# Optimization experiments

Hardware: AMD Instinct MI355X
Metric: run time of the kernel (lower is better)

Reference implementation:

```python
import jax, jax.numpy as jnp
import numpy as np

N0, N1, N2 = 100000, 20000, 4000
DEG = 10
G_NODES = 200000
D, ED, CD, FF, NHEAD = 512, 256, 300, 2048, 2


def _layernorm(x, g, b, eps=1e-5):
    m = jnp.mean(x, -1, keepdims=True)
    v = jnp.var(x, -1, keepdims=True)
    return (x - m) * jax.lax.rsqrt(v + eps) * g + b


def _mha(q_in, kv_in, w_in, b_in, w_out, b_out):
    # torch nn.MultiheadAttention, inputs are (seq, batch, d)
    d = q_in.shape[-1]
    wq, wk, wv = w_in[:d], w_in[d:2 * d], w_in[2 * d:]
    bq, bk, bv = b_in[:d], b_in[d:2 * d], b_in[2 * d:]
    dh = d // NHEAD
    q = (q_in @ wq.T + bq).reshape(q_in.shape[0], q_in.shape[1], NHEAD, dh)
    k = (kv_in @ wk.T + bk).reshape(kv_in.shape[0], kv_in.shape[1], NHEAD, dh)
    v = (kv_in @ wv.T + bv).reshape(kv_in.shape[0], kv_in.shape[1], NHEAD, dh)
    scores = jnp.einsum('qnhd,knhd->nhqk', q, k) * (dh ** -0.5)
    o = jnp.einsum('nhqk,knhd->qnhd', jax.nn.softmax(scores, -1), v)
    o = o.reshape(q_in.shape[0], q_in.shape[1], d)
    return o @ w_out.T + b_out


def setup_inputs() -> dict:
    key = jax.random.key(0)
    k = lambda i: jax.random.fold_in(key, i)
    inp = {}
    inp['nid0'] = jax.random.randint(k(0), (N0,), 0, G_NODES, dtype=jnp.int32)
    inp['nid1'] = jax.random.randint(k(1), (N1,), 0, G_NODES, dtype=jnp.int32)
    inp['nid2'] = jax.random.randint(k(2), (N2,), 0, G_NODES, dtype=jnp.int32)
    inp['esrc0'] = jax.random.randint(k(3), (N1 * DEG,), 0, N0, dtype=jnp.int32)
    inp['edst0'] = jnp.repeat(jnp.arange(N1, dtype=jnp.int32), DEG)
    inp['esrc1'] = jax.random.randint(k(4), (N2 * DEG,), 0, N1, dtype=jnp.int32)
    inp['edst1'] = jnp.repeat(jnp.arange(N2, dtype=jnp.int32), DEG)
    inp['content0'] = jax.random.normal(k(5), (N0, CD), jnp.float32)
    inp['content1'] = jax.random.normal(k(6), (N1, CD), jnp.float32)
    inp['content2'] = jax.random.normal(k(7), (N2, CD), jnp.float32)
    inp['node_emb_w'] = jax.random.normal(k(8), (G_NODES + 1, ED), jnp.float32) / ED
    inp['ee_w'] = jax.random.normal(k(9), (D, ED), jnp.float32) * 0.06
    inp['ee_b'] = jax.random.normal(k(10), (D,), jnp.float32) * 0.001
    inp['proj_w'] = jax.random.normal(k(11), (D, CD), jnp.float32) * 0.06
    inp['proj_b'] = jax.random.normal(k(12), (D,), jnp.float32) * 0.001
    inp['proj_g'] = jnp.ones((D,), jnp.float32)
    inp['proj_beta'] = jnp.zeros((D,), jnp.float32)
    L = 2  # decoder layers
    inp['sa_in_w'] = jax.random.normal(k(13), (L, 3 * D, D), jnp.float32) * 0.04
    inp['sa_in_b'] = jnp.zeros((L, 3 * D), jnp.float32)
    inp['sa_out_w'] = jax.random.normal(k(14), (L, D, D), jnp.float32) * 0.04
    inp['sa_out_b'] = jnp.zeros((L, D), jnp.float32)
    inp['ca_in_w'] = jax.random.normal(k(15), (L, 3 * D, D), jnp.float32) * 0.04
    inp['ca_in_b'] = jnp.zeros((L, 3 * D), jnp.float32)
    inp['ca_out_w'] = jax.random.normal(k(16), (L, D, D), jnp.float32) * 0.04
    inp['ca_out_b'] = jnp.zeros((L, D), jnp.float32)
    inp['lin1_w'] = jax.random.normal(k(17), (L, FF, D), jnp.float32) * 0.03
    inp['lin1_b'] = jnp.zeros((L, FF), jnp.float32)
    inp['lin2_w'] = jax.random.normal(k(18), (L, D, FF), jnp.float32) * 0.03
    inp['lin2_b'] = jnp.zeros((L, D), jnp.float32)
    for n in ('n1', 'n2', 'n3'):
        inp[n + '_g'] = jnp.ones((L, D), jnp.float32)
        inp[n + '_b'] = jnp.zeros((L, D), jnp.float32)
    return inp


def _forward(nid0, nid1, nid2, esrc0, edst0, esrc1, edst1,
             content0, content1, content2, node_emb_w, ee_w, ee_b,
             proj_w, proj_b, proj_g, proj_beta,
             sa_in_w, sa_in_b, sa_out_w, sa_out_b,
             ca_in_w, ca_in_b, ca_out_w, ca_out_b,
             lin1_w, lin1_b, lin2_w, lin2_b,
             n1_g, n1_b, n2_g, n2_b, n3_g, n3_b):
    def node_h(nid, content):
        nh = node_emb_w[nid + 1] @ ee_w.T + ee_b           # emb_expand(node_emb(nid+1))
        c = _layernorm(jax.nn.leaky_relu(content @ proj_w.T + proj_b, 0.1), proj_g, proj_beta)
        h = nh + c                                          # mix_embeddings (c[:, :D] == c)
        return h / jnp.maximum(jnp.linalg.norm(h, axis=1, keepdims=True), 1e-5)

    h0 = node_h(nid0, content0)
    h1 = node_h(nid1, content1)
    h2 = node_h(nid2, content2)

    def agg_mean(h_src, src, dst, n_dst):
        s = jax.ops.segment_sum(h_src[src], dst, num_segments=n_dst)
        w = jax.ops.segment_sum(jnp.ones(src.shape[0], h_src.dtype), dst, num_segments=n_dst)
        return s / w[:, None]

    # block 0: non-prediction GraphConv -> concat(mean_agg, h), L2 normalize
    m1 = agg_mean(h0, esrc0, edst0, N1)
    h1 = jnp.concatenate([m1, h1], axis=1)                  # (N1, 2D)
    h1 = h1 / jnp.maximum(jnp.linalg.norm(h1, axis=1, keepdims=True), 1e-5)

    # block 1: prediction GraphConv -> transformer-decoder fusion
    m2 = agg_mean(h1, esrc1, edst1, N2)                     # (N2, 2D)
    mem = m2.reshape(N2, 2, D).transpose(1, 0, 2)           # (n_layer=2, N2, D)
    tgt = h2[None]                                          # (1, N2, D)
    for l in range(2):  # post-norm TransformerDecoderLayer, gelu, dropout=0
        t2 = _mha(tgt, tgt, sa_in_w[l], sa_in_b[l], sa_out_w[l], sa_out_b[l])
        tgt = _layernorm(tgt + t2, n1_g[l], n1_b[l])
        t2 = _mha(tgt, mem, ca_in_w[l], ca_in_b[l], ca_out_w[l], ca_out_b[l])
        tgt = _layernorm(tgt + t2, n2_g[l], n2_b[l])
        ff = jax.nn.gelu(tgt @ lin1_w[l].T + lin1_b[l], approximate=False) @ lin2_w[l].T + lin2_b[l]
        tgt = _layernorm(tgt + ff, n3_g[l], n3_b[l])
    out = tgt[0]                                            # squeeze -> (N2, D)
    return out / jnp.maximum(jnp.linalg.norm(out, axis=1, keepdims=True), 1e-5)


def reference(nid0, nid1, nid2, esrc0, edst0, esrc1, edst1,
              content0, content1, content2, node_emb_w, ee_w, ee_b,
              proj_w, proj_b, proj_g, proj_beta,
              sa_in_w, sa_in_b, sa_out_w, sa_out_b,
              ca_in_w, ca_in_b, ca_out_w, ca_out_b,
              lin1_w, lin1_b, lin2_w, lin2_b,
              n1_g, n1_b, n2_g, n2_b, n3_g, n3_b):
    return _forward(nid0, nid1, nid2, esrc0, edst0, esrc1, edst1,
                    content0, content1, content2, node_emb_w, ee_w, ee_b,
                    proj_w, proj_b, proj_g, proj_beta,
                    sa_in_w, sa_in_b, sa_out_w, sa_out_b,
                    ca_in_w, ca_in_b, ca_out_w, ca_out_b,
                    lin1_w, lin1_b, lin2_w, lin2_b,
                    n1_g, n1_b, n2_g, n2_b, n3_g, n3_b)
```

## Files before the change

kernel.cpp:

```cpp
#include <hip/hip_runtime.h>
#include <math.h>

static constexpr int kN0  = 100000;
static constexpr int kN1  = 20000;
static constexpr int kN2  = 4000;
static constexpr int kDeg = 10;
static constexpr int kD   = 512;
static constexpr int kFF  = 2048;
static constexpr int kRows  = 48;
static constexpr int kRowsN = 32;
static constexpr int kLdA  = 584;
static constexpr int kLdG  = 520;

using short8  = __attribute__((ext_vector_type(8))) short;
using floatx4 = __attribute__((ext_vector_type(4))) float;

__device__ inline unsigned short f2bf(float f) {
    union { float f; unsigned u; } v; v.f = f;
    unsigned r = v.u + 0x7FFFu + ((v.u >> 16) & 1u);
    return (unsigned short)(r >> 16);
}
__device__ inline float bf2f(ushort u) {
    union { unsigned v; float f; } x; x.v = (unsigned)u << 16; return x.f;
}

__global__ __launch_bounds__(256) void pack_node_w_kernel(
    const float* __restrict__ ee_w, const float* __restrict__ proj_w,
    ushort* __restrict__ Bp)
{
    int tid  = blockIdx.x * 256 + threadIdx.x;
    int lane = tid & 63;
    int tile = tid >> 6;
    int n     = (tile & 31) * 16 + (lane & 15);
    int kbase = (tile >> 5) * 32 + (lane >> 4) * 8;
    ushort v[8];
    #pragma unroll
    for (int j = 0; j < 8; ++j) {
        int k = kbase + j;
        float f = 0.f;
        if (k < 256)      f = ee_w[(size_t)n * 256 + k];
        else if (k < 556) f = proj_w[(size_t)n * 300 + (k - 256)];
        v[j] = f2bf(f);
    }
    uint4 u;
    u.x = (unsigned)v[0] | ((unsigned)v[1] << 16);
    u.y = (unsigned)v[2] | ((unsigned)v[3] << 16);
    u.z = (unsigned)v[4] | ((unsigned)v[5] << 16);
    u.w = (unsigned)v[6] | ((unsigned)v[7] << 16);
    *(uint4*)(Bp + (size_t)tid * 8) = u;
}

__global__ __launch_bounds__(256) void pack512_many_kernel(
    const float* __restrict__ sa_in_w, const float* __restrict__ sa_out_w,
    const float* __restrict__ ca_in_w, const float* __restrict__ ca_out_w,
    ushort* __restrict__ dst)
{
    int y = blockIdx.y, l = y / 6, m = y % 6;
    const float* W;
    switch (m) {
        case 0: W = sa_in_w  + (size_t)l * 3 * kD * kD + (size_t)2 * kD * kD; break;
        case 1: W = sa_out_w + (size_t)l * kD * kD; break;
        case 2: W = ca_in_w  + (size_t)l * 3 * kD * kD; break;
        case 3: W = ca_in_w  + (size_t)l * 3 * kD * kD + (size_t)kD * kD; break;
        case 4: W = ca_in_w  + (size_t)l * 3 * kD * kD + (size_t)2 * kD * kD; break;
        default:W = ca_out_w + (size_t)l * kD * kD; break;
    }
    int tid  = blockIdx.x * 256 + threadIdx.x;
    int lane = tid & 63;
    int tile = tid >> 6;
    int n  = (tile & 31) * 16 + (lane & 15);
    int kb = (tile >> 5) * 32 + (lane >> 4) * 8;
    const float* src = W + (size_t)n * 512 + kb;
    ushort v[8];
    #pragma unroll
    for (int j = 0; j < 8; ++j) v[j] = f2bf(src[j]);
    uint4 u;
    u.x = (unsigned)v[0] | ((unsigned)v[1] << 16);
    u.y = (unsigned)v[2] | ((unsigned)v[3] << 16);
    u.z = (unsigned)v[4] | ((unsigned)v[5] << 16);
    u.w = (unsigned)v[6] | ((unsigned)v[7] << 16);
    *(uint4*)(dst + (size_t)y * 262144 + (size_t)tid * 8) = u;
}

__global__ __launch_bounds__(256) void pack_generic_kernel(
    const float* __restrict__ src, size_t srcStride,
    ushort* __restrict__ dst, size_t dstStride, int N, int K)
{
    int tid  = blockIdx.x * 256 + threadIdx.x;
    int NT = N >> 4;
    int lane = tid & 63;
    int tile = tid >> 6;
    int ct = tile % NT, kc = tile / NT;
    int n  = ct * 16 + (lane & 15);
    int kb = kc * 32 + (lane >> 4) * 8;
    const float* W = src + blockIdx.y * srcStride + (size_t)n * K + kb;
    ushort v[8];
    #pragma unroll
    for (int j = 0; j < 8; ++j) v[j] = f2bf(W[j]);
    uint4 u;
    u.x = (unsigned)v[0] | ((unsigned)v[1] << 16);
    u.y = (unsigned)v[2] | ((unsigned)v[3] << 16);
    u.z = (unsigned)v[4] | ((unsigned)v[5] << 16);
    u.w = (unsigned)v[6] | ((unsigned)v[7] << 16);
    *(uint4*)(dst + blockIdx.y * dstStride + (size_t)tid * 8) = u;
}

__global__ __launch_bounds__(512, 4) void node_h_mfma(
    const int* __restrict__ nid0a, const float* __restrict__ content0a,
    ushort* __restrict__ outB0, int n0,
    const int* __restrict__ nid1a, const float* __restrict__ content1a,
    ushort* __restrict__ outB1, int n1,
    const int* __restrict__ nid2a, const float* __restrict__ content2a,
    ushort* __restrict__ outB2, float* __restrict__ outF2, int n2,
    const float* __restrict__ node_emb_w,
    const ushort* __restrict__ Bp,
    const float* __restrict__ ee_b, const float* __restrict__ proj_b,
    const float* __restrict__ proj_g, const float* __restrict__ proj_beta)
{
    __shared__ __align__(16) ushort As[kRowsN * kLdA];
    __shared__ float redS[8][kRowsN], redQ[8][kRowsN];
    __shared__ float meanv[kRowsN], rstdv[kRowsN], rowinv[kRowsN];

    const int t    = threadIdx.x;
    const int lane = t & 63;
    const int wv   = t >> 6;
    const int quad = lane >> 4;
    const int l15  = lane & 15;

    const int g0 = (n0 + kRowsN - 1) / kRowsN;
    const int g1 = (n1 + kRowsN - 1) / kRowsN;
    int bx = blockIdx.x;
    const int* nid; const float* content; ushort* outB; float* outF = nullptr;
    int ldh, n;
    if (bx < g0)           { nid = nid0a; content = content0a; outB = outB0; ldh = 512;  n = n0; }
    else if (bx < g0 + g1) { bx -= g0; nid = nid1a; content = content1a; outB = outB1; ldh = 1024; n = n1; }
    else                   { bx -= g0 + g1; nid = nid2a; content = content2a; outB = outB2; outF = outF2; ldh = 512; n = n2; }
    const int row0 = bx * kRowsN;

    #pragma unroll
    for (int it = 0; it < 9; ++it) {
        int flat = it * 512 + t;
        int r  = flat / 144;
        int k4 = flat - r * 144;
        int row = row0 + r; if (row >= n) row = n - 1;
        float4 f = make_float4(0.f, 0.f, 0.f, 0.f);
        if (k4 < 64)
            f = *(const float4*)(node_emb_w + ((size_t)(nid[row] + 1)) * 256 + k4 * 4);
        else if (k4 < 139)
            f = *(const float4*)(content + (size_t)row * 300 + (k4 - 64) * 4);
        ushort4 o = make_ushort4(f2bf(f.x), f2bf(f.y), f2bf(f.z), f2bf(f.w));
        *(ushort4*)(As + (size_t)r * kLdA + k4 * 4) = o;
    }
    __syncthreads();

    floatx4 acc[2][4] = {};
    const short8* BpV = (const short8*)Bp;

    #pragma unroll
    for (int kc = 8; kc < 18; ++kc) {
        const short8* bp = BpV + (size_t)(kc * 32 + wv * 4) * 64 + lane;
        short8 b0 = bp[0], b1 = bp[64], b2 = bp[128], b3 = bp[192];
        short8 a[2];
        #pragma unroll
        for (int rt = 0; rt < 2; ++rt)
            a[rt] = *(const short8*)(As + (size_t)(rt * 16 + l15) * kLdA + kc * 32 + quad * 8);
        #pragma unroll
        for (int rt = 0; rt < 2; ++rt) {
            acc[rt][0] = __builtin_amdgcn_mfma_f32_16x16x32_bf16(a[rt], b0, acc[rt][0], 0, 0, 0);
            acc[rt][1] = __builtin_amdgcn_mfma_f32_16x16x32_bf16(a[rt], b1, acc[rt][1], 0, 0, 0);
            acc[rt][2] = __builtin_amdgcn_mfma_f32_16x16x32_bf16(a[rt], b2, acc[rt][2], 0, 0, 0);
            acc[rt][3] = __builtin_amdgcn_mfma_f32_16x16x32_bf16(a[rt], b3, acc[rt][3], 0, 0, 0);
        }
    }

    const int colbase = wv * 64 + l15;
    float pb[4], pg[4], pbt[4], eb[4];
    #pragma unroll
    for (int ct = 0; ct < 4; ++ct) {
        int c = colbase + ct * 16;
        pb[ct]  = proj_b[c];
        pg[ct]  = proj_g[c];
        pbt[ct] = proj_beta[c];
        eb[ct]  = ee_b[c];
    }

    float s8[8], q8[8];
    #pragma unroll
    for (int rt = 0; rt < 2; ++rt) {
        #pragma unroll
        for (int i = 0; i < 4; ++i) {
            float s = 0.f, q = 0.f;
            #pragma unroll
            for (int ct = 0; ct < 4; ++ct) {
                float c = acc[rt][ct][i] + pb[ct];
                c = (c >= 0.f) ? c : 0.1f * c;
                acc[rt][ct][i] = c;
                s += c; q = fmaf(c, c, q);
            }
            s8[rt * 4 + i] = s; q8[rt * 4 + i] = q;
        }
    }
    #pragma unroll
    for (int idx = 0; idx < 8; ++idx) {
        #pragma unroll
        for (int m = 1; m < 16; m <<= 1) {
            s8[idx] += __shfl_xor(s8[idx], m);
            q8[idx] += __shfl_xor(q8[idx], m);
        }
    }
    if (l15 == 0) {
        #pragma unroll
        for (int rt = 0; rt < 2; ++rt)
            #pragma unroll
            for (int i = 0; i < 4; ++i) {
                int rl = rt * 16 + quad * 4 + i;
                redS[wv][rl] = s8[rt * 4 + i];
                redQ[wv][rl] = q8[rt * 4 + i];
            }
    }
    __syncthreads();
    if (t < kRowsN) {
        float s = 0.f, q = 0.f;
        #pragma unroll
        for (int w = 0; w < 8; ++w) { s += redS[w][t]; q += redQ[w][t]; }
        float m   = s * (1.f / 512.f);
        float var = q * (1.f / 512.f) - m * m;
        meanv[t] = m;
        rstdv[t] = rsqrtf(var + 1e-5f);
    }
    __syncthreads();

    #pragma unroll
    for (int rt = 0; rt < 2; ++rt) {
        #pragma unroll
        for (int i = 0; i < 4; ++i) {
            int rl = rt * 16 + quad * 4 + i;
            float m = meanv[rl], rs = rstdv[rl];
            #pragma unroll
            for (int ct = 0; ct < 4; ++ct)
                acc[rt][ct][i] = (acc[rt][ct][i] - m) * rs * pg[ct] + pbt[ct] + eb[ct];
        }
    }

    #pragma unroll
    for (int kc = 0; kc < 8; ++kc) {
        const short8* bp = BpV + (size_t)(kc * 32 + wv * 4) * 64 + lane;
        short8 b0 = bp[0], b1 = bp[64], b2 = bp[128], b3 = bp[192];
        short8 a[2];
        #pragma unroll
        for (int rt = 0; rt < 2; ++rt)
            a[rt] = *(const short8*)(As + (size_t)(rt * 16 + l15) * kLdA + kc * 32 + quad * 8);
        #pragma unroll
        for (int rt = 0; rt < 2; ++rt) {
            acc[rt][0] = __builtin_amdgcn_mfma_f32_16x16x32_bf16(a[rt], b0, acc[rt][0], 0, 0, 0);
            acc[rt][1] = __builtin_amdgcn_mfma_f32_16x16x32_bf16(a[rt], b1, acc[rt][1], 0, 0, 0);
            acc[rt][2] = __builtin_amdgcn_mfma_f32_16x16x32_bf16(a[rt], b2, acc[rt][2], 0, 0, 0);
            acc[rt][3] = __builtin_amdgcn_mfma_f32_16x16x32_bf16(a[rt], b3, acc[rt][3], 0, 0, 0);
        }
    }

    #pragma unroll
    for (int rt = 0; rt < 2; ++rt) {
        #pragma unroll
        for (int i = 0; i < 4; ++i) {
            float psq = 0.f;
            #pragma unroll
            for (int ct = 0; ct < 4; ++ct)
                psq = fmaf(acc[rt][ct][i], acc[rt][ct][i], psq);
            q8[rt * 4 + i] = psq;
        }
    }
    #pragma unroll
    for (int idx = 0; idx < 8; ++idx)
        #pragma unroll
        for (int m = 1; m < 16; m <<= 1)
            q8[idx] += __shfl_xor(q8[idx], m);
    if (l15 == 0) {
        #pragma unroll
        for (int rt = 0; rt < 2; ++rt)
            #pragma unroll
            for (int i = 0; i < 4; ++i)
                redS[wv][rt * 16 + quad * 4 + i] = q8[rt * 4 + i];
    }
    __syncthreads();
    if (t < kRowsN) {
        float s = 0.f;
        #pragma unroll
        for (int w = 0; w < 8; ++w) s += redS[w][t];
        rowinv[t] = 1.f / fmaxf(sqrtf(s), 1e-5f);
    }
    __syncthreads();

    #pragma unroll
    for (int rt = 0; rt < 2; ++rt) {
        #pragma unroll
        for (int i = 0; i < 4; ++i) {
            int rl = rt * 16 + quad * 4 + i;
            int grow = row0 + rl;
            if (grow < n) {
                float inv = rowinv[rl];
                ushort* dB = outB + (size_t)grow * ldh + colbase;
                #pragma unroll
                for (int ct = 0; ct < 4; ++ct) {
                    float v = acc[rt][ct][i] * inv;
                    dB[ct * 16] = f2bf(v);
                    if (outF) outF[(size_t)grow * ldh + colbase + ct * 16] = v;
                }
            }
        }
    }
}

__device__ inline float gelu_exact(float x) {
    return 0.5f * x * (1.f + erff(x * 0.70710678118654752f));
}

template<int EPI>
__global__ __launch_bounds__(512, 2) void gemm_mfma(
    const ushort* __restrict__ A, int lda,
    const ushort* __restrict__ Bp, const float* __restrict__ bias,
    ushort* __restrict__ Cb, float* __restrict__ Cf, int ldc,
    const float* __restrict__ resid,
    const float* __restrict__ lng, const float* __restrict__ lnb,
    int M, int K, int N)
{
    __shared__ __align__(16) ushort As[kRows * kLdG];
    __shared__ float redS[8][kRows], redQ[8][kRows];
    __shared__ float meanv[kRows], rstdv[kRows];

    const int t    = threadIdx.x;
    const int lane = t & 63;
    const int wv   = t >> 6;
    const int quad = lane >> 4;
    const int l15  = lane & 15;
    const int row0 = blockIdx.x * kRows;
    const int nb   = blockIdx.y;
    const int NT   = N >> 4;

    floatx4 acc[3][4] = {};
    const short8* BpV = (const short8*)Bp;

    for (int k0 = 0; k0 < K; k0 += 512) {
        #pragma unroll
        for (int it = 0; it < 6; ++it) {
            int flat = it * 512 + t;
            int r  = flat >> 6;
            int k8 = flat & 63;
            int row = row0 + r; if (row >= M) row = M - 1;
            short8 v = *(const short8*)(A + (size_t)row * lda + k0 + k8 * 8);
            *(short8*)(As + (size_t)r * kLdG + k8 * 8) = v;
        }
        __syncthreads();
        const int g0 = k0 >> 5;
        #pragma unroll
        for (int kc = 0; kc < 16; ++kc) {
            const short8* bp = BpV + ((size_t)(g0 + kc) * NT + nb * 32 + wv * 4) * 64 + lane;
            short8 b0 = bp[0], b1 = bp[64], b2 = bp[128], b3 = bp[192];
            short8 a[3];
            #pragma unroll
            for (int rt = 0; rt < 3; ++rt)
                a[rt] = *(const short8*)(As + (size_t)(rt * 16 + l15) * kLdG + kc * 32 + quad * 8);
            #pragma unroll
            for (int rt = 0; rt < 3; ++rt) {
                acc[rt][0] = __builtin_amdgcn_mfma_f32_16x16x32_bf16(a[rt], b0, acc[rt][0], 0, 0, 0);
                acc[rt][1] = __builtin_amdgcn_mfma_f32_16x16x32_bf16(a[rt], b1, acc[rt][1], 0, 0, 0);
                acc[rt][2] = __builtin_amdgcn_mfma_f32_16x16x32_bf16(a[rt], b2, acc[rt][2], 0, 0, 0);
                acc[rt][3] = __builtin_amdgcn_mfma_f32_16x16x32_bf16(a[rt], b3, acc[rt][3], 0, 0, 0);
            }
        }
        __syncthreads();
    }

    const int colloc = wv * 64 + l15;
    float b[4];
    #pragma unroll
    for (int ct = 0; ct < 4; ++ct) b[ct] = bias[nb * 512 + colloc + ct * 16];

    if constexpr (EPI == 0 || EPI == 1) {
        #pragma unroll
        for (int rt = 0; rt < 3; ++rt) {
            #pragma unroll
            for (int i = 0; i < 4; ++i) {
                int row = row0 + rt * 16 + quad * 4 + i;
                if (row < M) {
                    ushort* dst = Cb + (size_t)row * ldc + nb * 512 + colloc;
                    #pragma unroll
                    for (int ct = 0; ct < 4; ++ct) {
                        float v = acc[rt][ct][i] + b[ct];
                        if (EPI == 1) v = gelu_exact(v);
                        dst[ct * 16] = f2bf(v);
                    }
                }
            }
        }
    } else {
        float lg[4], lb[4];
        #pragma unroll
        for (int ct = 0; ct < 4; ++ct) {
            lg[ct] = lng[colloc + ct * 16];
            lb[ct] = lnb[colloc + ct * 16];
        }
        float s12[12], q12[12];
        #pragma unroll
        for (int rt = 0; rt < 3; ++rt) {
            #pragma unroll
            for (int i = 0; i < 4; ++i) {
                int rl = rt * 16 + quad * 4 + i;
                int row = row0 + rl; if (row >= M) row = M - 1;
                const float* rr = resid + (size_t)row * 512 + colloc;
                float s = 0.f, q = 0.f;
                #pragma unroll
                for (int ct = 0; ct < 4; ++ct) {
                    float h = acc[rt][ct][i] + b[ct] + rr[ct * 16];
                    acc[rt][ct][i] = h;
                    s += h; q = fmaf(h, h, q);
                }
                s12[rt * 4 + i] = s; q12[rt * 4 + i] = q;
            }
        }
        #pragma unroll
        for (int idx = 0; idx < 12; ++idx) {
            #pragma unroll
            for (int m = 1; m < 16; m <<= 1) {
                s12[idx] += __shfl_xor(s12[idx], m);
                q12[idx] += __shfl_xor(q12[idx], m);
            }
        }
        if (l15 == 0) {
            #pragma unroll
            for (int rt = 0; rt < 3; ++rt)
                #pragma unroll
                for (int i = 0; i < 4; ++i) {
                    int rl = rt * 16 + quad * 4 + i;
                    redS[wv][rl] = s12[rt * 4 + i];
                    redQ[wv][rl] = q12[rt * 4 + i];
                }
        }
        __syncthreads();
        if (t < kRows) {
            float s = 0.f, q = 0.f;
            #pragma unroll
            for (int w = 0; w < 8; ++w) { s += redS[w][t]; q += redQ[w][t]; }
            float m   = s * (1.f / 512.f);
            float var = q * (1.f / 512.f) - m * m;
            meanv[t] = m;
            rstdv[t] = rsqrtf(var + 1e-5f);
        }
        __syncthreads();
        #pragma unroll
        for (int rt = 0; rt < 3; ++rt) {
            #pragma unroll
            for (int i = 0; i < 4; ++i) {
                int rl = rt * 16 + quad * 4 + i;
                int row = row0 + rl;
                if (row < M) {
                    float m = meanv[rl], rs = rstdv[rl];
                    float*  dF = Cf + (size_t)row * 512 + colloc;
                    ushort* dB = Cb + (size_t)row * 512 + colloc;
                    #pragma unroll
                    for (int ct = 0; ct < 4; ++ct) {
                        float v = (acc[rt][ct][i] - m) * rs * lg[ct] + lb[ct];
                        dF[ct * 16] = v;
                        dB[ct * 16] = f2bf(v);
                    }
                }
            }
        }
    }
}

__global__ __launch_bounds__(512, 2) void gemm3_mfma(
    const ushort* __restrict__ A0, const ushort* __restrict__ B0,
    const float* __restrict__ b0p, ushort* __restrict__ C0, int M0,
    const ushort* __restrict__ A1, const ushort* __restrict__ B1,
    const float* __restrict__ b1p, ushort* __restrict__ C1, int M1,
    const ushort* __restrict__ A2, const ushort* __restrict__ B2,
    const float* __restrict__ b2p, ushort* __restrict__ C2, int M2)
{
    __shared__ __align__(16) ushort As[kRows * kLdG];

    const int t    = threadIdx.x;
    const int lane = t & 63;
    const int wv   = t >> 6;
    const int quad = lane >> 4;
    const int l15  = lane & 15;

    const int g0 = (M0 + kRows - 1) / kRows;
    const int g1 = (M1 + kRows - 1) / kRows;
    int bx = blockIdx.x;
    const ushort* A; const ushort* Bw; const float* bias; ushort* C; int M;
    if (bx < g0)           { A = A0; Bw = B0; bias = b0p; C = C0; M = M0; }
    else if (bx < g0 + g1) { bx -= g0; A = A1; Bw = B1; bias = b1p; C = C1; M = M1; }
    else                   { bx -= g0 + g1; A = A2; Bw = B2; bias = b2p; C = C2; M = M2; }
    const int row0 = bx * kRows;

    floatx4 acc[3][4] = {};
    const short8* BpV = (const short8*)Bw;

    #pragma unroll
    for (int it = 0; it < 6; ++it) {
        int flat = it * 512 + t;
        int r  = flat >> 6;
        int k8 = flat & 63;
        int row = row0 + r; if (row >= M) row = M - 1;
        short8 v = *(const short8*)(A + (size_t)row * 512 + k8 * 8);
        *(short8*)(As + (size_t)r * kLdG + k8 * 8) = v;
    }
    __syncthreads();
    #pragma unroll
    for (int kc = 0; kc < 16; ++kc) {
        const short8* bp = BpV + ((size_t)kc * 32 + wv * 4) * 64 + lane;
        short8 b0 = bp[0], b1 = bp[64], b2 = bp[128], b3 = bp[192];
        short8 a[3];
        #pragma unroll
        for (int rt = 0; rt < 3; ++rt)
            a[rt] = *(const short8*)(As + (size_t)(rt * 16 + l15) * kLdG + kc * 32 + quad * 8);
        #pragma unroll
        for (int rt = 0; rt < 3; ++rt) {
            acc[rt][0] = __builtin_amdgcn_mfma_f32_16x16x32_bf16(a[rt], b0, acc[rt][0], 0, 0, 0);
            acc[rt][1] = __builtin_amdgcn_mfma_f32_16x16x32_bf16(a[rt], b1, acc[rt][1], 0, 0, 0);
            acc[rt][2] = __builtin_amdgcn_mfma_f32_16x16x32_bf16(a[rt], b2, acc[rt][2], 0, 0, 0);
            acc[rt][3] = __builtin_amdgcn_mfma_f32_16x16x32_bf16(a[rt], b3, acc[rt][3], 0, 0, 0);
        }
    }

    const int colloc = wv * 64 + l15;
    float b[4];
    #pragma unroll
    for (int ct = 0; ct < 4; ++ct) b[ct] = bias[colloc + ct * 16];
    #pragma unroll
    for (int rt = 0; rt < 3; ++rt) {
        #pragma unroll
        for (int i = 0; i < 4; ++i) {
            int row = row0 + rt * 16 + quad * 4 + i;
            if (row < M) {
                ushort* dst = C + (size_t)row * 512 + colloc;
                #pragma unroll
                for (int ct = 0; ct < 4; ++ct)
                    dst[ct * 16] = f2bf(acc[rt][ct][i] + b[ct]);
            }
        }
    }
}

__device__ inline float block_sum256(float v, float* red4) {
    #pragma unroll
    for (int off = 32; off > 0; off >>= 1) v += __shfl_down(v, off);
    if ((threadIdx.x & 63) == 0) red4[threadIdx.x >> 6] = v;
    __syncthreads();
    return red4[0] + red4[1] + red4[2] + red4[3];
}

__global__ __launch_bounds__(256) void agg_norm1_kernel(
    const ushort* __restrict__ h0, const int* __restrict__ esrc,
    ushort* __restrict__ h1cat)
{
    __shared__ int idx[kDeg];
    __shared__ float red4[4];
    int i = blockIdx.x, t = threadIdx.x;
    if (t < kDeg) idx[t] = esrc[i * kDeg + t];
    __syncthreads();
    float s0 = 0.f, s1 = 0.f;
    for (int e = 0; e < kDeg; ++e) {
        const ushort* hr = h0 + (size_t)idx[e] * 512;
        s0 += bf2f(hr[t]); s1 += bf2f(hr[t + 256]);
    }
    s0 *= 0.1f; s1 *= 0.1f;
    size_t base = (size_t)i * 1024;
    float o0 = bf2f(h1cat[base + 512 + t]);
    float o1 = bf2f(h1cat[base + 768 + t]);
    float tot = block_sum256(s0 * s0 + s1 * s1 + o0 * o0 + o1 * o1, red4);
    float inv = 1.f / fmaxf(sqrtf(tot), 1e-5f);
    h1cat[base + t]       = f2bf(s0 * inv);
    h1cat[base + 256 + t] = f2bf(s1 * inv);
    h1cat[base + 512 + t] = f2bf(o0 * inv);
    h1cat[base + 768 + t] = f2bf(o1 * inv);
}

__global__ __launch_bounds__(256) void agg2_kernel(
    const ushort* __restrict__ h1cat, const int* __restrict__ esrc,
    ushort* __restrict__ m2)
{
    __shared__ int idx[kDeg];
    int i = blockIdx.x, t = threadIdx.x;
    if (t < kDeg) idx[t] = esrc[i * kDeg + t];
    __syncthreads();
    float s0 = 0.f, s1 = 0.f, s2 = 0.f, s3 = 0.f;
    for (int e = 0; e < kDeg; ++e) {
        const ushort* hr = h1cat + (size_t)idx[e] * 1024;
        s0 += bf2f(hr[t]);       s1 += bf2f(hr[t + 256]);
        s2 += bf2f(hr[t + 512]); s3 += bf2f(hr[t + 768]);
    }
    size_t base = (size_t)i * 1024;
    m2[base + t]       = f2bf(s0 * 0.1f);
    m2[base + 256 + t] = f2bf(s1 * 0.1f);
    m2[base + 512 + t] = f2bf(s2 * 0.1f);
    m2[base + 768 + t] = f2bf(s3 * 0.1f);
}

__global__ __launch_bounds__(256) void attn_combine_kernel(
    const ushort* __restrict__ Q,
    const ushort* __restrict__ Kb, const ushort* __restrict__ Vb,
    ushort* __restrict__ O)
{
    __shared__ float red[4][4];
    __shared__ float a[4];
    int i = blockIdx.x, t = threadIdx.x;
    size_t base  = (size_t)i * 512;
    size_t base0 = (size_t)(2 * i) * 512;
    size_t base1 = base0 + 512;
    float q0 = bf2f(Q[base + t]), q1 = bf2f(Q[base + t + 256]);
    float p00 = q0 * bf2f(Kb[base0 + t]);
    float p01 = q0 * bf2f(Kb[base1 + t]);
    float p10 = q1 * bf2f(Kb[base0 + t + 256]);
    float p11 = q1 * bf2f(Kb[base1 + t + 256]);
    #pragma unroll
    for (int off = 32; off > 0; off >>= 1) {
        p00 += __shfl_down(p00, off);
        p01 += __shfl_down(p01, off);
        p10 += __shfl_down(p10, off);
        p11 += __shfl_down(p11, off);
    }
    int w = t >> 6;
    if ((t & 63) == 0) { red[w][0] = p00; red[w][1] = p01; red[w][2] = p10; red[w][3] = p11; }
    __syncthreads();
    if (t == 0) {
        float s00 = (red[0][0] + red[1][0] + red[2][0] + red[3][0]) * 0.0625f;
        float s01 = (red[0][1] + red[1][1] + red[2][1] + red[3][1]) * 0.0625f;
        float s10 = (red[0][2] + red[1][2] + red[2][2] + red[3][2]) * 0.0625f;
        float s11 = (red[0][3] + red[1][3] + red[2][3] + red[3][3]) * 0.0625f;
        float m0 = fmaxf(s00, s01);
        float e0 = expf(s00 - m0), e1 = expf(s01 - m0);
        float d0 = e0 + e1;
        a[0] = e0 / d0; a[1] = e1 / d0;
        float m1 = fmaxf(s10, s11);
        float f0 = expf(s10 - m1), f1 = expf(s11 - m1);
        float d1 = f0 + f1;
        a[2] = f0 / d1; a[3] = f1 / d1;
    }
    __syncthreads();
    O[base + t]       = f2bf(a[0] * bf2f(Vb[base0 + t])       + a[1] * bf2f(Vb[base1 + t]));
    O[base + t + 256] = f2bf(a[2] * bf2f(Vb[base0 + t + 256]) + a[3] * bf2f(Vb[base1 + t + 256]));
}

__global__ __launch_bounds__(256) void final_norm_kernel(
    const float* __restrict__ tgt, float* __restrict__ out)
{
    __shared__ float red4[4];
    int i = blockIdx.x, t = threadIdx.x;
    size_t base = (size_t)i * 512;
    float v0 = tgt[base + t], v1 = tgt[base + t + 256];
    float tot = block_sum256(v0 * v0 + v1 * v1, red4);
    float inv = 1.f / fmaxf(sqrtf(tot), 1e-5f);
    out[base + t]       = v0 * inv;
    out[base + t + 256] = v1 * inv;
}

extern "C" void kernel_launch(void* const* d_in, const int* in_sizes, int n_in,
                              void* d_out, int out_size, void* d_ws, size_t ws_size,
                              hipStream_t stream)
{
    (void)in_sizes; (void)n_in; (void)out_size; (void)ws_size;
    const int*   nid0       = (const int*)d_in[0];
    const int*   nid1       = (const int*)d_in[1];
    const int*   nid2       = (const int*)d_in[2];
    const int*   esrc0      = (const int*)d_in[3];
    const int*   esrc1      = (const int*)d_in[5];
    const float* content0   = (const float*)d_in[7];
    const float* content1   = (const float*)d_in[8];
    const float* content2   = (const float*)d_in[9];
    const float* node_emb_w = (const float*)d_in[10];
    const float* ee_w       = (const float*)d_in[11];
    const float* ee_b       = (const float*)d_in[12];
    const float* proj_w     = (const float*)d_in[13];
    const float* proj_b     = (const float*)d_in[14];
    const float* proj_g     = (const float*)d_in[15];
    const float* proj_beta  = (const float*)d_in[16];
    const float* sa_in_w    = (const float*)d_in[17];
    const float* sa_in_b    = (const float*)d_in[18];
    const float* sa_out_w   = (const float*)d_in[19];
    const float* sa_out_b   = (const float*)d_in[20];
    const float* ca_in_w    = (const float*)d_in[21];
    const float* ca_in_b    = (const float*)d_in[22];
    const float* ca_out_w   = (const float*)d_in[23];
    const float* ca_out_b   = (const float*)d_in[24];
    const float* lin1_w     = (const float*)d_in[25];
    const float* lin1_b     = (const float*)d_in[26];
    const float* lin2_w     = (const float*)d_in[27];
    const float* lin2_b     = (const float*)d_in[28];
    const float* n1_g       = (const float*)d_in[29];
    const float* n1_b       = (const float*)d_in[30];
    const float* n2_g       = (const float*)d_in[31];
    const float* n2_b       = (const float*)d_in[32];
    const float* n3_g       = (const float*)d_in[33];
    const float* n3_b       = (const float*)d_in[34];

    float* ws = (float*)d_ws;
    size_t off = 0;
    ushort* h0b    = (ushort*)(ws + off); off += (size_t)kN0 * 512 / 2;
    ushort* h1catb = (ushort*)(ws + off); off += (size_t)kN1 * 1024 / 2;
    ushort* m2b    = (ushort*)(ws + off); off += (size_t)kN2 * 1024 / 2;
    float*  tgt    = ws + off;            off += (size_t)kN2 * 512;
    ushort* tgtb   = (ushort*)(ws + off); off += (size_t)kN2 * 512 / 2;
    ushort* Qbb    = (ushort*)(ws + off); off += (size_t)kN2 * 512 / 2;
    ushort* Kbb    = (ushort*)(ws + off); off += (size_t)2 * kN2 * 512 / 2;
    ushort* Vbb    = (ushort*)(ws + off); off += (size_t)2 * kN2 * 512 / 2;
    ushort* Obb    = (ushort*)(ws + off); off += (size_t)kN2 * 512 / 2;
    ushort* ffhb   = (ushort*)(ws + off); off += (size_t)kN2 * 2048 / 2;
    ushort* BpNode = (ushort*)(ws + off); off += 147456;
    ushort* Pw512  = (ushort*)(ws + off); off += 12 * 262144 / 2;
    ushort* Pl1    = (ushort*)(ws + off); off += 2 * 1048576 / 2;
    ushort* Pl2    = (ushort*)(ws + off); off += 2 * 1048576 / 2;

    dim3 blk(256);

    pack_node_w_kernel<<<dim3(144), blk, 0, stream>>>(ee_w, proj_w, BpNode);
    pack512_many_kernel<<<dim3(128, 12), blk, 0, stream>>>(
        sa_in_w, sa_out_w, ca_in_w, ca_out_w, Pw512);
    pack_generic_kernel<<<dim3(512, 2), blk, 0, stream>>>(
        lin1_w, (size_t)kFF * kD, Pl1, 1048576, kFF, kD);
    pack_generic_kernel<<<dim3(512, 2), blk, 0, stream>>>(
        lin2_w, (size_t)kD * kFF, Pl2, 1048576, kD, kFF);

    {
        int g0 = (kN0 + kRowsN - 1) / kRowsN;
        int g1 = (kN1 + kRowsN - 1) / kRowsN;
        int g2 = (kN2 + kRowsN - 1) / kRowsN;
        node_h_mfma<<<dim3(g0 + g1 + g2), dim3(512), 0, stream>>>(
            nid0, content0, h0b, kN0,
            nid1, content1, h1catb + 512, kN1,
            nid2, content2, tgtb, tgt, kN2,
            node_emb_w, BpNode, ee_b, proj_b, proj_g, proj_beta);
    }

    agg_norm1_kernel<<<dim3(kN1), blk, 0, stream>>>(h0b, esrc0, h1catb);
    agg2_kernel<<<dim3(kN2), blk, 0, stream>>>(h1catb, esrc1, m2b);

    const int M   = kN2;
    const int gM  = (M + kRows - 1) / kRows;
    const int gM2 = (2 * M + kRows - 1) / kRows;
    dim3 blk512(512);
    for (int l = 0; l < 2; ++l) {
        const ushort* sa_v_p   = Pw512 + (size_t)(l * 6 + 0) * 262144;
        const ushort* sa_out_p = Pw512 + (size_t)(l * 6 + 1) * 262144;
        const ushort* ca_q_p   = Pw512 + (size_t)(l * 6 + 2) * 262144;
        const ushort* ca_k_p   = Pw512 + (size_t)(l * 6 + 3) * 262144;
        const ushort* ca_v_p   = Pw512 + (size_t)(l * 6 + 4) * 262144;
        const ushort* ca_out_p = Pw512 + (size_t)(l * 6 + 5) * 262144;
        const ushort* l1_p     = Pl1 + (size_t)l * 1048576;
        const ushort* l2_p     = Pl2 + (size_t)l * 1048576;
        const float* sa_b = sa_in_b + (size_t)l * 3 * kD;
        const float* saob = sa_out_b + (size_t)l * kD;
        const float* ca_b = ca_in_b + (size_t)l * 3 * kD;
        const float* caob = ca_out_b + (size_t)l * kD;
        const float* l1b = lin1_b + (size_t)l * kFF;
        const float* l2b = lin2_b + (size_t)l * kD;

        gemm3_mfma<<<dim3(gM + gM2 + gM2), blk512, 0, stream>>>(
            tgtb, sa_v_p, sa_b + 2 * kD, Qbb, M,
            m2b,  ca_k_p, ca_b + kD,     Kbb, 2 * M,
            m2b,  ca_v_p, ca_b + 2 * kD, Vbb, 2 * M);

        gemm_mfma<2><<<dim3(gM, 1), blk512, 0, stream>>>(
            Qbb, 512, sa_out_p, saob, tgtb, tgt, 512,
            tgt, n1_g + l * kD, n1_b + l * kD, M, 512, 512);

        gemm_mfma<0><<<dim3(gM, 1), blk512, 0, stream>>>(
            tgtb, 512, ca_q_p, ca_b, Qbb, nullptr, 512,
            nullptr, nullptr, nullptr, M, 512, 512);
        attn_combine_kernel<<<dim3(M), blk, 0, stream>>>(Qbb, Kbb, Vbb, Obb);
        gemm_mfma<2><<<dim3(gM, 1), blk512, 0, stream>>>(
            Obb, 512, ca_out_p, caob, tgtb, tgt, 512,
            tgt, n2_g + l * kD, n2_b + l * kD, M, 512, 512);

        gemm_mfma<1><<<dim3(gM, 4), blk512, 0, stream>>>(
            tgtb, 512, l1_p, l1b, ffhb, nullptr, 2048,
            nullptr, nullptr, nullptr, M, 512, 2048);
        gemm_mfma<2><<<dim3(gM, 1), blk512, 0, stream>>>(
            ffhb, 2048, l2_p, l2b, tgtb, tgt, 512,
            tgt, n3_g + l * kD, n3_b + l * kD, M, 2048, 512);
    }

    final_norm_kernel<<<dim3(kN2), blk, 0, stream>>>(tgt, (float*)d_out);
}
```

Measured before the change: 961.0 us.

## Fuse follow-on projections into LayerNorm GEMM epilogues and hoist cross-attn K/V

Adds an EPI==3 variant of the GEMM. After the LayerNorm epilogue it writes the normalised bf16 row tile into shared memory and multiplies it by a second 512x512 weight, producing the next projection (cross-attn Q, or the next layer's self-attn V) in the same launch. Cross-attention K/V for both layers depend only on m2b, so they are computed once up front in a single 5-way batched GEMM launch. The node_h_mfma launch bound is raised to 8 waves per SIMD. Together these cut kernel launches and re-reads of tgtb, at the cost of extra buffers and more register pressure from the second accumulator.

```diff
diff --git a/kernel.cpp b/kernel.cpp
--- a/kernel.cpp
+++ b/kernel.cpp
@@ -105,7 +105,7 @@
     *(uint4*)(dst + blockIdx.y * dstStride + (size_t)tid * 8) = u;
 }
 
-__global__ __launch_bounds__(512, 4) void node_h_mfma(
+__global__ __launch_bounds__(512, 8) void node_h_mfma(
     const int* __restrict__ nid0a, const float* __restrict__ content0a,
     ushort* __restrict__ outB0, int n0,
     const int* __restrict__ nid1a, const float* __restrict__ content1a,
@@ -322,7 +322,9 @@
     ushort* __restrict__ Cb, float* __restrict__ Cf, int ldc,
     const float* __restrict__ resid,
     const float* __restrict__ lng, const float* __restrict__ lnb,
-    int M, int K, int N)
+    int M, int K, int N,
+    const ushort* __restrict__ Bp2, const float* __restrict__ bias2,
+    ushort* __restrict__ C2)
 {
     __shared__ __align__(16) ushort As[kRows * kLdG];
     __shared__ float redS[8][kRows], redQ[8][kRows];
@@ -462,20 +464,63 @@
                         float v = (acc[rt][ct][i] - m) * rs * lg[ct] + lb[ct];
                         dF[ct * 16] = v;
                         dB[ct * 16] = f2bf(v);
+                        if (EPI == 3)
+                            As[(size_t)rl * kLdG + colloc + ct * 16] = f2bf(v);
                     }
                 }
             }
         }
-    }
-}
-
-__global__ __launch_bounds__(512, 2) void gemm3_mfma(
-    const ushort* __restrict__ A0, const ushort* __restrict__ B0,
+        if constexpr (EPI == 3) {
+            __syncthreads();
+            floatx4 acc2[3][4] = {};
+            const short8* Bp2V = (const short8*)Bp2;
+            #pragma unroll
+            for (int kc = 0; kc < 16; ++kc) {
+                const short8* bp = Bp2V + ((size_t)kc * 32 + wv * 4) * 64 + lane;
+                short8 b0 = bp[0], b1 = bp[64], b2 = bp[128], b3 = bp[192];
+                short8 a[3];
+                #pragma unroll
+                for (int rt = 0; rt < 3; ++rt)
+                    a[rt] = *(const short8*)(As + (size_t)(rt * 16 + l15) * kLdG + kc * 32 + quad * 8);
+                #pragma unroll
+                for (int rt = 0; rt < 3; ++rt) {
+                    acc2[rt][0] = __builtin_amdgcn_mfma_f32_16x16x32_bf16(a[rt], b0, acc2[rt][0], 0, 0, 0);
+                    acc2[rt][1] = __builtin_amdgcn_mfma_f32_16x16x32_bf16(a[rt], b1, acc2[rt][1], 0, 0, 0);
+                    acc2[rt][2] = __builtin_amdgcn_mfma_f32_16x16x32_bf16(a[rt], b2, acc2[rt][2], 0, 0, 0);
+                    acc2[rt][3] = __builtin_amdgcn_mfma_f32_16x16x32_bf16(a[rt], b3, acc2[rt][3], 0, 0, 0);
+                }
+            }
+            float b2[4];
+            #pragma unroll
+            for (int ct = 0; ct < 4; ++ct) b2[ct] = bias2[colloc + ct * 16];
+            #pragma unroll
+            for (int rt = 0; rt < 3; ++rt) {
+                #pragma unroll
+                for (int i = 0; i < 4; ++i) {
+                    int row = row0 + rt * 16 + quad * 4 + i;
+                    if (row < M) {
+                        ushort* dst = C2 + (size_t)row * 512 + colloc;
+                        #pragma unroll
+                        for (int ct = 0; ct < 4; ++ct)
+                            dst[ct * 16] = f2bf(acc2[rt][ct][i] + b2[ct]);
+                    }
+                }
+            }
+        }
+    }
+}
+
+__global__ __launch_bounds__(512, 2) void gemm5_mfma(
+    const ushort* __restrict__ A0, const ushort* __restrict__ B0w,
     const float* __restrict__ b0p, ushort* __restrict__ C0, int M0,
-    const ushort* __restrict__ A1, const ushort* __restrict__ B1,
+    const ushort* __restrict__ A1, const ushort* __restrict__ B1w,
     const float* __restrict__ b1p, ushort* __restrict__ C1, int M1,
-    const ushort* __restrict__ A2, const ushort* __restrict__ B2,
-    const float* __restrict__ b2p, ushort* __restrict__ C2, int M2)
+    const ushort* __restrict__ A2, const ushort* __restrict__ B2w,
+    const float* __restrict__ b2p, ushort* __restrict__ C2, int M2,
+    const ushort* __restrict__ A3, const ushort* __restrict__ B3w,
+    const float* __restrict__ b3p, ushort* __restrict__ C3, int M3,
+    const ushort* __restrict__ A4, const ushort* __restrict__ B4w,
+    const float* __restrict__ b4p, ushort* __restrict__ C4, int M4)
 {
     __shared__ __align__(16) ushort As[kRows * kLdG];
 
@@ -487,11 +532,15 @@
 
     const int g0 = (M0 + kRows - 1) / kRows;
     const int g1 = (M1 + kRows - 1) / kRows;
+    const int g2 = (M2 + kRows - 1) / kRows;
+    const int g3 = (M3 + kRows - 1) / kRows;
     int bx = blockIdx.x;
     const ushort* A; const ushort* Bw; const float* bias; ushort* C; int M;
-    if (bx < g0)           { A = A0; Bw = B0; bias = b0p; C = C0; M = M0; }
-    else if (bx < g0 + g1) { bx -= g0; A = A1; Bw = B1; bias = b1p; C = C1; M = M1; }
-    else                   { bx -= g0 + g1; A = A2; Bw = B2; bias = b2p; C = C2; M = M2; }
+    if (bx < g0)                { A = A0; Bw = B0w; bias = b0p; C = C0; M = M0; }
+    else if (bx < g0+g1)        { bx -= g0;       A = A1; Bw = B1w; bias = b1p; C = C1; M = M1; }
+    else if (bx < g0+g1+g2)     { bx -= g0+g1;    A = A2; Bw = B2w; bias = b2p; C = C2; M = M2; }
+    else if (bx < g0+g1+g2+g3)  { bx -= g0+g1+g2; A = A3; Bw = B3w; bias = b3p; C = C3; M = M3; }
+    else                        { bx -= g0+g1+g2+g3; A = A4; Bw = B4w; bias = b4p; C = C4; M = M4; }
     const int row0 = bx * kRows;
 
     floatx4 acc[3][4] = {};
@@ -703,8 +752,10 @@
     float*  tgt    = ws + off;            off += (size_t)kN2 * 512;
     ushort* tgtb   = (ushort*)(ws + off); off += (size_t)kN2 * 512 / 2;
     ushort* Qbb    = (ushort*)(ws + off); off += (size_t)kN2 * 512 / 2;
-    ushort* Kbb    = (ushort*)(ws + off); off += (size_t)2 * kN2 * 512 / 2;
-    ushort* Vbb    = (ushort*)(ws + off); off += (size_t)2 * kN2 * 512 / 2;
+    ushort* Kb0    = (ushort*)(ws + off); off += (size_t)2 * kN2 * 512 / 2;
+    ushort* Vb0    = (ushort*)(ws + off); off += (size_t)2 * kN2 * 512 / 2;
+    ushort* Kb1    = (ushort*)(ws + off); off += (size_t)2 * kN2 * 512 / 2;
+    ushort* Vb1    = (ushort*)(ws + off); off += (size_t)2 * kN2 * 512 / 2;
     ushort* Obb    = (ushort*)(ws + off); off += (size_t)kN2 * 512 / 2;
     ushort* ffhb   = (ushort*)(ws + off); off += (size_t)kN2 * 2048 / 2;
     ushort* BpNode = (ushort*)(ws + off); off += 147456;
@@ -740,45 +791,56 @@
     const int gM  = (M + kRows - 1) / kRows;
     const int gM2 = (2 * M + kRows - 1) / kRows;
     dim3 blk512(512);
+
+    gemm5_mfma<<<dim3(gM + 4 * gM2), blk512, 0, stream>>>(
+        tgtb, Pw512 + (size_t)0 * 262144, sa_in_b + 2 * kD,              Qbb, M,
+        m2b,  Pw512 + (size_t)3 * 262144, ca_in_b + kD,                  Kb0, 2 * M,
+        m2b,  Pw512 + (size_t)4 * 262144, ca_in_b + 2 * kD,              Vb0, 2 * M,
+        m2b,  Pw512 + (size_t)9 * 262144, ca_in_b + 3 * kD + kD,         Kb1, 2 * M,
+        m2b,  Pw512 + (size_t)10 * 262144, ca_in_b + 3 * kD + 2 * kD,    Vb1, 2 * M);
+
     for (int l = 0; l < 2; ++l) {
-        const ushort* sa_v_p   = Pw512 + (size_t)(l * 6 + 0) * 262144;
         const ushort* sa_out_p = Pw512 + (size_t)(l * 6 + 1) * 262144;
         const ushort* ca_q_p   = Pw512 + (size_t)(l * 6 + 2) * 262144;
-        const ushort* ca_k_p   = Pw512 + (size_t)(l * 6 + 3) * 262144;
-        const ushort* ca_v_p   = Pw512 + (size_t)(l * 6 + 4) * 262144;
         const ushort* ca_out_p = Pw512 + (size_t)(l * 6 + 5) * 262144;
         const ushort* l1_p     = Pl1 + (size_t)l * 1048576;
         const ushort* l2_p     = Pl2 + (size_t)l * 1048576;
-        const float* sa_b = sa_in_b + (size_t)l * 3 * kD;
         const float* saob = sa_out_b + (size_t)l * kD;
         const float* ca_b = ca_in_b + (size_t)l * 3 * kD;
         const float* caob = ca_out_b + (size_t)l * kD;
         const float* l1b = lin1_b + (size_t)l * kFF;
         const float* l2b = lin2_b + (size_t)l * kD;
-
-        gemm3_mfma<<<dim3(gM + gM2 + gM2), blk512, 0, stream>>>(
-            tgtb, sa_v_p, sa_b + 2 * kD, Qbb, M,
-            m2b,  ca_k_p, ca_b + kD,     Kbb, 2 * M,
-            m2b,  ca_v_p, ca_b + 2 * kD, Vbb, 2 * M);
-
-        gemm_mfma<2><<<dim3(gM, 1), blk512, 0, stream>>>(
+        const ushort* Kb_l = (l == 0) ? Kb0 : Kb1;
+        const ushort* Vb_l = (l == 0) ? Vb0 : Vb1;
+
+        gemm_mfma<3><<<dim3(gM, 1), blk512, 0, stream>>>(
             Qbb, 512, sa_out_p, saob, tgtb, tgt, 512,
-            tgt, n1_g + l * kD, n1_b + l * kD, M, 512, 512);
-
-        gemm_mfma<0><<<dim3(gM, 1), blk512, 0, stream>>>(
-            tgtb, 512, ca_q_p, ca_b, Qbb, nullptr, 512,
-            nullptr, nullptr, nullptr, M, 512, 512);
-        attn_combine_kernel<<<dim3(M), blk, 0, stream>>>(Qbb, Kbb, Vbb, Obb);
+            tgt, n1_g + l * kD, n1_b + l * kD, M, 512, 512,
+            ca_q_p, ca_b, Qbb);
+
+        attn_combine_kernel<<<dim3(M), blk, 0, stream>>>(Qbb, Kb_l, Vb_l, Obb);
+
         gemm_mfma<2><<<dim3(gM, 1), blk512, 0, stream>>>(
             Obb, 512, ca_out_p, caob, tgtb, tgt, 512,
-            tgt, n2_g + l * kD, n2_b + l * kD, M, 512, 512);
+            tgt, n2_g + l * kD, n2_b + l * kD, M, 512, 512,
+            nullptr, nullptr, nullptr);
 
         gemm_mfma<1><<<dim3(gM, 4), blk512, 0, stream>>>(
             tgtb, 512, l1_p, l1b, ffhb, nullptr, 2048,
-            nullptr, nullptr, nullptr, M, 512, 2048);
-        gemm_mfma<2><<<dim3(gM, 1), blk512, 0, stream>>>(
-            ffhb, 2048, l2_p, l2b, tgtb, tgt, 512,
-            tgt, n3_g + l * kD, n3_b + l * kD, M, 2048, 512);
+            nullptr, nullptr, nullptr, M, 512, 2048,
+            nullptr, nullptr, nullptr);
+
+        if (l == 0) {
+            gemm_mfma<3><<<dim3(gM, 1), blk512, 0, stream>>>(
+                ffhb, 2048, l2_p, l2b, tgtb, tgt, 512,
+                tgt, n3_g + l * kD, n3_b + l * kD, M, 2048, 512,
+                Pw512 + (size_t)(6 + 0) * 262144, sa_in_b + 3 * kD + 2 * kD, Qbb);
+        } else {
+            gemm_mfma<2><<<dim3(gM, 1), blk512, 0, stream>>>(
+                ffhb, 2048, l2_p, l2b, tgtb, tgt, 512,
+                tgt, n3_g + l * kD, n3_b + l * kD, M, 2048, 512,
+                nullptr, nullptr, nullptr);
+        }
     }
 
     final_norm_kernel<<<dim3(kN2), blk, 0, stream>>>(tgt, (float*)d_out);
```

Measured after the change: 1.164 ms. 21.1% more time.
